# Kernel optimization log

Hardware: AMD Instinct MI355X
Metric: run time of the kernel (lower is better)

## Reference

```python
import jax, jax.numpy as jnp
import numpy as np

N_NODES = 50000
N_EDGES = 800000
N_NODE_DICT = 10000
N_EDGE_DICT = 100
EMB = 128
HID = 32
HEADS = 4
SLOPE = 0.2
LN_EPS = 1e-5


def layer_norm(x, gamma, beta):
    mu = jnp.mean(x, axis=-1, keepdims=True)
    var = jnp.mean(jnp.square(x - mu), axis=-1, keepdims=True)
    return (x - mu) * jax.lax.rsqrt(var + LN_EPS) * gamma + beta


def setup_inputs() -> dict:
    key = jax.random.key(0)
    ks = jax.random.split(key, 10)
    D = HID * HEADS
    inp = {
        "node_features": jax.random.randint(ks[0], (N_NODES,), 0, N_NODE_DICT),
        "edge_features": jax.random.randint(ks[1], (N_EDGES,), 0, N_EDGE_DICT),
        "edge_index": jax.random.randint(ks[2], (2, N_EDGES), 0, N_NODES),
        "node_emb": jax.random.normal(ks[3], (N_NODE_DICT, EMB), jnp.float32),
        "edge_emb": jax.random.normal(ks[4], (N_EDGE_DICT, EMB), jnp.float32),
        "w_W": jax.random.normal(ks[5], (EMB, D), jnp.float32) / np.sqrt(EMB),
        "w_b": jnp.zeros((D,), jnp.float32),
        "ew_W": jax.random.normal(ks[6], (EMB, D), jnp.float32) / np.sqrt(EMB),
        "ew_b": jnp.zeros((D,), jnp.float32),
        "attn": jax.random.normal(ks[7], (HEADS, 3 * HID), jnp.float32) * 0.1,
        "ln_gamma": jnp.ones((D,), jnp.float32),
        "ln_beta": jnp.zeros((D,), jnp.float32),
    }
    return inp


def reference(node_features, edge_features, edge_index, node_emb, edge_emb,
              w_W, w_b, ew_W, ew_b, attn, ln_gamma, ln_beta):
    # embedding lookups
    nf = node_emb[node_features]                       # [N, EMB]
    ef = edge_emb[edge_features]                       # [E, EMB]
    # linear projections -> [*, heads, hid]
    h = (nf @ w_W + w_b).reshape(-1, HEADS, HID)       # [N, H, F]
    eh = (ef @ ew_W + ew_b).reshape(-1, HEADS, HID)    # [E, H, F]
    tgt = edge_index[0]
    src = edge_index[1]
    # attn = [a_i || a_j || a_e]; dot with concat == sum of per-part dots
    a_i, a_j, a_e = attn[:, :HID], attn[:, HID:2 * HID], attn[:, 2 * HID:]
    s_i = jnp.einsum('nhf,hf->nh', h, a_i)             # [N, H]
    s_j = jnp.einsum('nhf,hf->nh', h, a_j)             # [N, H]
    s_e = jnp.einsum('ehf,hf->eh', eh, a_e)            # [E, H]
    eij = jax.nn.leaky_relu(s_i[tgt] + s_j[src] + s_e, negative_slope=SLOPE)  # [E, H]
    # scatter softmax over edges grouped by target node
    m = jax.ops.segment_max(eij, tgt, num_segments=N_NODES)   # [N, H]
    ex = jnp.exp(eij - m[tgt])
    denom = jax.ops.segment_sum(ex, tgt, num_segments=N_NODES)
    alpha = ex / denom[tgt]                            # [E, H]
    # message passing + scatter_add
    message = alpha[..., None] * h[src]                # [E, H, F]
    out = jax.ops.segment_sum(message, tgt, num_segments=N_NODES)  # [N, H, F]
    out = out + h                                      # skip connection
    out = out.reshape(-1, HEADS * HID)                 # concat heads
    eh2 = eh.reshape(-1, HEADS * HID)
    out = layer_norm(out, ln_gamma, ln_beta)
    eh2 = layer_norm(eh2, ln_gamma, ln_beta)
    return out, eh2
```

## Files before the change

kernel.cpp:

```cpp
#include <hip/hip_runtime.h>

#define NNODES 50000
#define NEDGES 800000
#define NNODE_DICT 10000
#define NEDGE_DICT 100
#define EMB 128
#define HID 32
#define HEADS 4
#define DD 128
#define SLOPE 0.2f
#define LN_EPS 1e-5f
#define NEG_BIG -3.0e38f

typedef float vfloat4 __attribute__((ext_vector_type(4)));

__global__ __launch_bounds__(128) void node_dict_kernel(
        const float* __restrict__ node_emb,
        const float* __restrict__ w_W,
        const float* __restrict__ w_b,
        const float* __restrict__ attn,
        float* __restrict__ h_dict,
        float* __restrict__ s_i_d,
        float* __restrict__ s_j_d) {
    __shared__ float a_rows[4][EMB];
    int r0 = blockIdx.x * 4;
    int col = threadIdx.x;
    #pragma unroll
    for (int r = 0; r < 4; ++r) a_rows[r][col] = node_emb[(r0 + r) * EMB + col];
    __syncthreads();
    float acc0 = 0.f, acc1 = 0.f, acc2 = 0.f, acc3 = 0.f;
    #pragma unroll 8
    for (int k = 0; k < EMB; ++k) {
        float wv = w_W[k * DD + col];
        acc0 += a_rows[0][k] * wv;
        acc1 += a_rows[1][k] * wv;
        acc2 += a_rows[2][k] * wv;
        acc3 += a_rows[3][k] * wv;
    }
    float b = w_b[col];
    acc0 += b; acc1 += b; acc2 += b; acc3 += b;
    h_dict[(r0 + 0) * DD + col] = acc0;
    h_dict[(r0 + 1) * DD + col] = acc1;
    h_dict[(r0 + 2) * DD + col] = acc2;
    h_dict[(r0 + 3) * DD + col] = acc3;

    int head = col >> 5, f = col & 31;
    float ai = attn[head * 96 + f];
    float aj = attn[head * 96 + 32 + f];
    float accs[4] = {acc0, acc1, acc2, acc3};
    #pragma unroll
    for (int r = 0; r < 4; ++r) {
        float pi = accs[r] * ai;
        float pj = accs[r] * aj;
        #pragma unroll
        for (int off = 16; off > 0; off >>= 1) {
            pi += __shfl_down(pi, off);
            pj += __shfl_down(pj, off);
        }
        if ((col & 31) == 0) {
            s_i_d[(r0 + r) * HEADS + head] = pi;
            s_j_d[(r0 + r) * HEADS + head] = pj;
        }
    }
}

__global__ void edge_dict_kernel(const float* __restrict__ edge_emb,
                                 const float* __restrict__ ew_W,
                                 const float* __restrict__ ew_b,
                                 const float* __restrict__ attn,
                                 const float* __restrict__ gamma,
                                 const float* __restrict__ beta,
                                 float* __restrict__ eh2_dict,
                                 float* __restrict__ s_e_d) {
    __shared__ float a_row[EMB];
    __shared__ float red[4];
    int row = blockIdx.x;
    int col = threadIdx.x;
    a_row[col] = edge_emb[row * EMB + col];
    __syncthreads();
    float acc = 0.f;
    #pragma unroll 8
    for (int k = 0; k < EMB; ++k) acc += a_row[k] * ew_W[k * DD + col];
    acc += ew_b[col];

    int head = col >> 5, f = col & 31;
    float pe = acc * attn[head * 96 + 64 + f];
    #pragma unroll
    for (int off = 16; off > 0; off >>= 1) pe += __shfl_down(pe, off);
    if ((col & 31) == 0) s_e_d[row * HEADS + head] = pe;

    float s = acc, s2 = acc * acc;
    #pragma unroll
    for (int off = 32; off > 0; off >>= 1) {
        s  += __shfl_down(s, off);
        s2 += __shfl_down(s2, off);
    }
    int wid = col >> 6;
    if ((col & 63) == 0) { red[wid * 2] = s; red[wid * 2 + 1] = s2; }
    __syncthreads();
    s = red[0] + red[2];
    s2 = red[1] + red[3];
    float mu = s * (1.f / DD);
    float var = s2 * (1.f / DD) - mu * mu;
    float r = rsqrtf(var + LN_EPS);
    eh2_dict[row * DD + col] = (acc - mu) * r * gamma[col] + beta[col];
}

__global__ void count_kernel(const int* __restrict__ edge_index,
                             int* __restrict__ counts) {
    int i = blockIdx.x * blockDim.x + threadIdx.x;
    if (i >= NEDGES / 4) return;
    int4 t = ((const int4*)edge_index)[i];
    atomicAdd(&counts[t.x], 1);
    atomicAdd(&counts[t.y], 1);
    atomicAdd(&counts[t.z], 1);
    atomicAdd(&counts[t.w], 1);
}

__global__ __launch_bounds__(256) void scan_tiles(const int* __restrict__ counts,
                                                  int* __restrict__ excl,
                                                  int* __restrict__ tsums) {
    __shared__ int wred[4];
    int tile = blockIdx.x;
    int tid = threadIdx.x;
    int base = tile * 1024 + tid * 4;
    int4 v = make_int4(0, 0, 0, 0);
    if (base + 3 < NNODES) {
        v = *(const int4*)(counts + base);
    } else {
        if (base + 0 < NNODES) v.x = counts[base + 0];
        if (base + 1 < NNODES) v.y = counts[base + 1];
        if (base + 2 < NNODES) v.z = counts[base + 2];
        if (base + 3 < NNODES) v.w = counts[base + 3];
    }
    int tsum = v.x + v.y + v.z + v.w;
    int lane = tid & 63, w = tid >> 6;
    int incl = tsum;
    #pragma unroll
    for (int o = 1; o < 64; o <<= 1) {
        int t = __shfl_up(incl, o);
        if (lane >= o) incl += t;
    }
    if (lane == 63) wred[w] = incl;
    __syncthreads();
    int wexc = 0;
    #pragma unroll
    for (int j = 0; j < 4; ++j) if (j < w) wexc += wred[j];
    int ex = wexc + incl - tsum;
    int4 o4 = make_int4(ex, ex + v.x, ex + v.x + v.y, ex + v.x + v.y + v.z);
    if (base + 3 < NNODES) {
        *(int4*)(excl + base) = o4;
    } else {
        if (base + 0 < NNODES) excl[base + 0] = o4.x;
        if (base + 1 < NNODES) excl[base + 1] = o4.y;
        if (base + 2 < NNODES) excl[base + 2] = o4.z;
        if (base + 3 < NNODES) excl[base + 3] = o4.w;
    }
    if (tid == 255) tsums[tile] = wexc + incl;
}

__global__ void scan_sums(int* __restrict__ tsums, int ntiles,
                          int* __restrict__ total) {
    int lane = threadIdx.x;
    int v = (lane < ntiles) ? tsums[lane] : 0;
    int incl = v;
    #pragma unroll
    for (int o = 1; o < 64; o <<= 1) {
        int t = __shfl_up(incl, o);
        if (lane >= o) incl += t;
    }
    if (lane < ntiles) tsums[lane] = incl - v;
    if (lane == 63) *total = incl;
}

__global__ void scan_fixup(const int* __restrict__ tsums,
                           int* __restrict__ offsets,
                           int* __restrict__ cursor) {
    int i = blockIdx.x * blockDim.x + threadIdx.x;
    if (i >= NNODES) return;
    int v = offsets[i] + tsums[i >> 10];
    offsets[i] = v;
    cursor[i] = v;
}

__global__ void scatter_kernel(const int* __restrict__ edge_index,
                               const int* __restrict__ node_features,
                               const int* __restrict__ edge_features,
                               int* __restrict__ cursor,
                               int2* __restrict__ csr) {
    int e = blockIdx.x * blockDim.x + threadIdx.x;
    if (e >= NEDGES) return;
    int tgt = edge_index[e];
    int src = edge_index[NEDGES + e];
    int ns = node_features[src];
    int ee = edge_features[e];
    int pos = atomicAdd(&cursor[tgt], 1);
    csr[pos] = make_int2(ns, ee);
}

__global__ __launch_bounds__(256) void node_agg_kernel(
        const int* __restrict__ offsets,
        const int2* __restrict__ csr,
        const int* __restrict__ node_features,
        const float4* __restrict__ s_i4,
        const float4* __restrict__ s_j4,
        const float4* __restrict__ s_e4,
        const float* __restrict__ h_dict,
        const float* __restrict__ gamma,
        const float* __restrict__ beta,
        float* __restrict__ out) {
    __shared__ float sp[4][256];
    __shared__ int   sns[4][64];
    int wid = threadIdx.x >> 6;
    int lane = threadIdx.x & 63;
    int n = blockIdx.x * 4 + wid;
    if (n >= NNODES) return;

    int nt = node_features[n];
    float4 si = s_i4[nt];
    int off = offsets[n];
    int deg = offsets[n + 1] - off;

    float m0 = NEG_BIG, m1 = NEG_BIG, m2 = NEG_BIG, m3 = NEG_BIG;
    float l0 = 0.f, l1 = 0.f, l2 = 0.f, l3 = 0.f;
    float acc0 = 0.f, acc1 = 0.f;
    int h0 = lane >> 5;
    int h1 = 2 + (lane >> 5);

    for (int base = 0; base < deg; base += 64) {
        int cnt = min(deg - base, 64);
        float4 ev = make_float4(NEG_BIG, NEG_BIG, NEG_BIG, NEG_BIG);
        int ns = 0;
        if (lane < cnt) {
            int2 pr = csr[off + base + lane];
            ns = pr.x;
            float4 sj = s_j4[pr.x];
            float4 se = s_e4[pr.y];
            ev.x = si.x + sj.x + se.x; ev.x = ev.x > 0.f ? ev.x : SLOPE * ev.x;
            ev.y = si.y + sj.y + se.y; ev.y = ev.y > 0.f ? ev.y : SLOPE * ev.y;
            ev.z = si.z + sj.z + se.z; ev.z = ev.z > 0.f ? ev.z : SLOPE * ev.z;
            ev.w = si.w + sj.w + se.w; ev.w = ev.w > 0.f ? ev.w : SLOPE * ev.w;
        }
        float4 mv = ev;
        #pragma unroll
        for (int o = 32; o > 0; o >>= 1) {
            mv.x = fmaxf(mv.x, __shfl_xor(mv.x, o));
            mv.y = fmaxf(mv.y, __shfl_xor(mv.y, o));
            mv.z = fmaxf(mv.z, __shfl_xor(mv.z, o));
            mv.w = fmaxf(mv.w, __shfl_xor(mv.w, o));
        }
        float nm0 = fmaxf(m0, mv.x), nm1 = fmaxf(m1, mv.y);
        float nm2 = fmaxf(m2, mv.z), nm3 = fmaxf(m3, mv.w);
        float4 p = make_float4(0.f, 0.f, 0.f, 0.f);
        if (lane < cnt) {
            p.x = __expf(ev.x - nm0);
            p.y = __expf(ev.y - nm1);
            p.z = __expf(ev.z - nm2);
            p.w = __expf(ev.w - nm3);
        }
        float4 sv = p;
        #pragma unroll
        for (int o = 32; o > 0; o >>= 1) {
            sv.x += __shfl_xor(sv.x, o);
            sv.y += __shfl_xor(sv.y, o);
            sv.z += __shfl_xor(sv.z, o);
            sv.w += __shfl_xor(sv.w, o);
        }
        float sc0 = __expf(m0 - nm0), sc1 = __expf(m1 - nm1);
        float sc2 = __expf(m2 - nm2), sc3 = __expf(m3 - nm3);
        l0 = l0 * sc0 + sv.x; l1 = l1 * sc1 + sv.y;
        l2 = l2 * sc2 + sv.z; l3 = l3 * sc3 + sv.w;
        m0 = nm0; m1 = nm1; m2 = nm2; m3 = nm3;
        acc0 *= (lane < 32) ? sc0 : sc1;
        acc1 *= (lane < 32) ? sc2 : sc3;
        if (lane < cnt) {
            sp[wid][lane * 4 + 0] = p.x;
            sp[wid][lane * 4 + 1] = p.y;
            sp[wid][lane * 4 + 2] = p.z;
            sp[wid][lane * 4 + 3] = p.w;
            sns[wid][lane] = ns;
        }
        int nst = sns[wid][0];
        for (int t = 0; t < cnt; ++t) {
            const float* hr = h_dict + (size_t)nst * DD;
            float w0 = sp[wid][t * 4 + h0];
            float w1 = sp[wid][t * 4 + h1];
            if (t + 1 < cnt) nst = sns[wid][t + 1];
            acc0 += w0 * hr[lane];
            acc1 += w1 * hr[lane + 64];
        }
    }

    float den0 = (lane < 32) ? l0 : l1;
    float den1 = (lane < 32) ? l2 : l3;
    float msg0 = den0 > 0.f ? acc0 / den0 : 0.f;
    float msg1 = den1 > 0.f ? acc1 / den1 : 0.f;
    const float* hres = h_dict + (size_t)nt * DD;
    float v0 = msg0 + hres[lane];
    float v1 = msg1 + hres[lane + 64];
    float s = v0 + v1, s2 = v0 * v0 + v1 * v1;
    #pragma unroll
    for (int o = 32; o > 0; o >>= 1) {
        s  += __shfl_xor(s, o);
        s2 += __shfl_xor(s2, o);
    }
    float mu = s * (1.f / DD);
    float var = s2 * (1.f / DD) - mu * mu;
    float r = rsqrtf(var + LN_EPS);
    out[(size_t)n * DD + lane]      = (v0 - mu) * r * gamma[lane] + beta[lane];
    out[(size_t)n * DD + lane + 64] = (v1 - mu) * r * gamma[lane + 64] + beta[lane + 64];
}

__global__ void edge_out_kernel(const int* __restrict__ edge_features,
                                const vfloat4* __restrict__ eh2_dict4,
                                vfloat4* __restrict__ out4) {
    int t = blockIdx.x * blockDim.x + threadIdx.x;
    int e = t >> 5;
    int j = t & 31;
    if (e >= NEDGES) return;
    int ee = edge_features[e];
    vfloat4 v = eh2_dict4[ee * 32 + j];
    __builtin_nontemporal_store(v, out4 + (size_t)t);
}

extern "C" void kernel_launch(void* const* d_in, const int* in_sizes, int n_in,
                              void* d_out, int out_size, void* d_ws, size_t ws_size,
                              hipStream_t stream) {
    const int*   node_features = (const int*)d_in[0];
    const int*   edge_features = (const int*)d_in[1];
    const int*   edge_index    = (const int*)d_in[2];
    const float* node_emb      = (const float*)d_in[3];
    const float* edge_emb      = (const float*)d_in[4];
    const float* w_W           = (const float*)d_in[5];
    const float* w_b           = (const float*)d_in[6];
    const float* ew_W          = (const float*)d_in[7];
    const float* ew_b          = (const float*)d_in[8];
    const float* attn          = (const float*)d_in[9];
    const float* gamma         = (const float*)d_in[10];
    const float* beta          = (const float*)d_in[11];

    float* out_nodes = (float*)d_out;
    float* out_edges = (float*)d_out + (size_t)NNODES * DD;

    char* w = (char*)d_ws;
    float* h_dict   = (float*)w;  w += (size_t)NNODE_DICT * DD * 4;
    float* s_i_d    = (float*)w;  w += (size_t)NNODE_DICT * 4 * 4;
    float* s_j_d    = (float*)w;  w += (size_t)NNODE_DICT * 4 * 4;
    float* eh2_dict = (float*)w;  w += (size_t)NEDGE_DICT * DD * 4;
    float* s_e_d    = (float*)w;  w += (size_t)NEDGE_DICT * 4 * 4;
    int*   counts   = (int*)w;    w += (size_t)NNODES * 4;
    int*   offsets  = (int*)w;    w += (size_t)(NNODES + 4) * 4;
    int*   cursor   = (int*)w;    w += (size_t)NNODES * 4;
    int*   tsums    = (int*)w;    w += (size_t)64 * 4;
    int2*  csr      = (int2*)w;   w += (size_t)NEDGES * 8;

    const int ntiles = (NNODES + 1023) / 1024;

    (void)hipMemsetAsync(counts, 0, (size_t)NNODES * 4, stream);

    node_dict_kernel<<<NNODE_DICT / 4, 128, 0, stream>>>(node_emb, w_W, w_b, attn,
                                                         h_dict, s_i_d, s_j_d);
    edge_dict_kernel<<<NEDGE_DICT, 128, 0, stream>>>(edge_emb, ew_W, ew_b, attn,
                                                     gamma, beta, eh2_dict, s_e_d);
    count_kernel<<<(NEDGES / 4 + 255) / 256, 256, 0, stream>>>(edge_index, counts);
    scan_tiles<<<ntiles, 256, 0, stream>>>(counts, offsets, tsums);
    scan_sums<<<1, 64, 0, stream>>>(tsums, ntiles, offsets + NNODES);
    scan_fixup<<<(NNODES + 255) / 256, 256, 0, stream>>>(tsums, offsets, cursor);
    scatter_kernel<<<(NEDGES + 255) / 256, 256, 0, stream>>>(edge_index, node_features,
                                                             edge_features, cursor, csr);
    node_agg_kernel<<<(NNODES + 3) / 4, 256, 0, stream>>>(offsets, csr, node_features,
                                                          (const float4*)s_i_d,
                                                          (const float4*)s_j_d,
                                                          (const float4*)s_e_d,
                                                          h_dict, gamma, beta, out_nodes);
    edge_out_kernel<<<(NEDGES * 32 + 255) / 256, 256, 0, stream>>>(edge_features,
                                                                   (const vfloat4*)eh2_dict,
                                                                   (vfloat4*)out_edges);
}
```

Baseline: 600.3 us.

## Merge independent kernels into front/back launches and fold scan_sums into fixup

Combines the node-dict, edge-dict and edge-count work into one launch that dispatches on block ID. It folds the tile-sum scan into the fixup kernel, where every block redundantly rescans the 49 tile sums. It also interleaves edge-output copy blocks with node-aggregation blocks (1 agg block per 8 copy blocks) in a single back kernel. The aim is fewer launches and overlap of the memory-bound edge copy with the latency-bound aggregation, at the cost of branch-heavy kernels whose resource usage is set by the larger path.

```diff
diff --git a/kernel.cpp b/kernel.cpp
--- a/kernel.cpp
+++ b/kernel.cpp
@@ -12,109 +12,117 @@
 #define LN_EPS 1e-5f
 #define NEG_BIG -3.0e38f
 
+#define NDICT_BLOCKS (NNODE_DICT / 4)
+#define EDICT_BLOCKS (NEDGE_DICT)
+#define COUNT_BLOCKS ((NEDGES / 4 + 127) / 128)
+#define NTILES ((NNODES + 1023) / 1024)
+#define AGG_BLOCKS ((NNODES + 3) / 4)
+#define EOUT_BLOCKS (NEDGES * 32 / 256)
+#define BACK_BLOCKS (AGG_BLOCKS + EOUT_BLOCKS)
+
 typedef float vfloat4 __attribute__((ext_vector_type(4)));
 
-__global__ __launch_bounds__(128) void node_dict_kernel(
+__global__ __launch_bounds__(128) void front_kernel(
         const float* __restrict__ node_emb,
         const float* __restrict__ w_W,
         const float* __restrict__ w_b,
         const float* __restrict__ attn,
         float* __restrict__ h_dict,
         float* __restrict__ s_i_d,
-        float* __restrict__ s_j_d) {
-    __shared__ float a_rows[4][EMB];
-    int r0 = blockIdx.x * 4;
+        float* __restrict__ s_j_d,
+        const float* __restrict__ edge_emb,
+        const float* __restrict__ ew_W,
+        const float* __restrict__ ew_b,
+        const float* __restrict__ gamma,
+        const float* __restrict__ beta,
+        float* __restrict__ eh2_dict,
+        float* __restrict__ s_e_d,
+        const int* __restrict__ edge_index,
+        int* __restrict__ counts) {
+    __shared__ float a_sh[4][EMB];
+    __shared__ float red[4];
+    int bid = blockIdx.x;
     int col = threadIdx.x;
-    #pragma unroll
-    for (int r = 0; r < 4; ++r) a_rows[r][col] = node_emb[(r0 + r) * EMB + col];
-    __syncthreads();
-    float acc0 = 0.f, acc1 = 0.f, acc2 = 0.f, acc3 = 0.f;
-    #pragma unroll 8
-    for (int k = 0; k < EMB; ++k) {
-        float wv = w_W[k * DD + col];
-        acc0 += a_rows[0][k] * wv;
-        acc1 += a_rows[1][k] * wv;
-        acc2 += a_rows[2][k] * wv;
-        acc3 += a_rows[3][k] * wv;
-    }
-    float b = w_b[col];
-    acc0 += b; acc1 += b; acc2 += b; acc3 += b;
-    h_dict[(r0 + 0) * DD + col] = acc0;
-    h_dict[(r0 + 1) * DD + col] = acc1;
-    h_dict[(r0 + 2) * DD + col] = acc2;
-    h_dict[(r0 + 3) * DD + col] = acc3;
-
-    int head = col >> 5, f = col & 31;
-    float ai = attn[head * 96 + f];
-    float aj = attn[head * 96 + 32 + f];
-    float accs[4] = {acc0, acc1, acc2, acc3};
-    #pragma unroll
-    for (int r = 0; r < 4; ++r) {
-        float pi = accs[r] * ai;
-        float pj = accs[r] * aj;
-        #pragma unroll
-        for (int off = 16; off > 0; off >>= 1) {
-            pi += __shfl_down(pi, off);
-            pj += __shfl_down(pj, off);
-        }
-        if ((col & 31) == 0) {
-            s_i_d[(r0 + r) * HEADS + head] = pi;
-            s_j_d[(r0 + r) * HEADS + head] = pj;
-        }
-    }
-}
-
-__global__ void edge_dict_kernel(const float* __restrict__ edge_emb,
-                                 const float* __restrict__ ew_W,
-                                 const float* __restrict__ ew_b,
-                                 const float* __restrict__ attn,
-                                 const float* __restrict__ gamma,
-                                 const float* __restrict__ beta,
-                                 float* __restrict__ eh2_dict,
-                                 float* __restrict__ s_e_d) {
-    __shared__ float a_row[EMB];
-    __shared__ float red[4];
-    int row = blockIdx.x;
-    int col = threadIdx.x;
-    a_row[col] = edge_emb[row * EMB + col];
-    __syncthreads();
-    float acc = 0.f;
-    #pragma unroll 8
-    for (int k = 0; k < EMB; ++k) acc += a_row[k] * ew_W[k * DD + col];
-    acc += ew_b[col];
-
-    int head = col >> 5, f = col & 31;
-    float pe = acc * attn[head * 96 + 64 + f];
-    #pragma unroll
-    for (int off = 16; off > 0; off >>= 1) pe += __shfl_down(pe, off);
-    if ((col & 31) == 0) s_e_d[row * HEADS + head] = pe;
-
-    float s = acc, s2 = acc * acc;
-    #pragma unroll
-    for (int off = 32; off > 0; off >>= 1) {
-        s  += __shfl_down(s, off);
-        s2 += __shfl_down(s2, off);
-    }
-    int wid = col >> 6;
-    if ((col & 63) == 0) { red[wid * 2] = s; red[wid * 2 + 1] = s2; }
-    __syncthreads();
-    s = red[0] + red[2];
-    s2 = red[1] + red[3];
-    float mu = s * (1.f / DD);
-    float var = s2 * (1.f / DD) - mu * mu;
-    float r = rsqrtf(var + LN_EPS);
-    eh2_dict[row * DD + col] = (acc - mu) * r * gamma[col] + beta[col];
-}
-
-__global__ void count_kernel(const int* __restrict__ edge_index,
-                             int* __restrict__ counts) {
-    int i = blockIdx.x * blockDim.x + threadIdx.x;
-    if (i >= NEDGES / 4) return;
-    int4 t = ((const int4*)edge_index)[i];
-    atomicAdd(&counts[t.x], 1);
-    atomicAdd(&counts[t.y], 1);
-    atomicAdd(&counts[t.z], 1);
-    atomicAdd(&counts[t.w], 1);
+
+    if (bid < NDICT_BLOCKS) {
+        int r0 = bid * 4;
+        #pragma unroll
+        for (int r = 0; r < 4; ++r) a_sh[r][col] = node_emb[(r0 + r) * EMB + col];
+        __syncthreads();
+        float acc0 = 0.f, acc1 = 0.f, acc2 = 0.f, acc3 = 0.f;
+        #pragma unroll 8
+        for (int k = 0; k < EMB; ++k) {
+            float wv = w_W[k * DD + col];
+            acc0 += a_sh[0][k] * wv;
+            acc1 += a_sh[1][k] * wv;
+            acc2 += a_sh[2][k] * wv;
+            acc3 += a_sh[3][k] * wv;
+        }
+        float b = w_b[col];
+        acc0 += b; acc1 += b; acc2 += b; acc3 += b;
+        h_dict[(r0 + 0) * DD + col] = acc0;
+        h_dict[(r0 + 1) * DD + col] = acc1;
+        h_dict[(r0 + 2) * DD + col] = acc2;
+        h_dict[(r0 + 3) * DD + col] = acc3;
+
+        int head = col >> 5, f = col & 31;
+        float ai = attn[head * 96 + f];
+        float aj = attn[head * 96 + 32 + f];
+        float accs[4] = {acc0, acc1, acc2, acc3};
+        #pragma unroll
+        for (int r = 0; r < 4; ++r) {
+            float pi = accs[r] * ai;
+            float pj = accs[r] * aj;
+            #pragma unroll
+            for (int off = 16; off > 0; off >>= 1) {
+                pi += __shfl_down(pi, off);
+                pj += __shfl_down(pj, off);
+            }
+            if ((col & 31) == 0) {
+                s_i_d[(r0 + r) * HEADS + head] = pi;
+                s_j_d[(r0 + r) * HEADS + head] = pj;
+            }
+        }
+    } else if (bid < NDICT_BLOCKS + EDICT_BLOCKS) {
+        int row = bid - NDICT_BLOCKS;
+        a_sh[0][col] = edge_emb[row * EMB + col];
+        __syncthreads();
+        float acc = 0.f;
+        #pragma unroll 8
+        for (int k = 0; k < EMB; ++k) acc += a_sh[0][k] * ew_W[k * DD + col];
+        acc += ew_b[col];
+
+        int head = col >> 5, f = col & 31;
+        float pe = acc * attn[head * 96 + 64 + f];
+        #pragma unroll
+        for (int off = 16; off > 0; off >>= 1) pe += __shfl_down(pe, off);
+        if ((col & 31) == 0) s_e_d[row * HEADS + head] = pe;
+
+        float s = acc, s2 = acc * acc;
+        #pragma unroll
+        for (int off = 32; off > 0; off >>= 1) {
+            s  += __shfl_down(s, off);
+            s2 += __shfl_down(s2, off);
+        }
+        int wid = col >> 6;
+        if ((col & 63) == 0) { red[wid * 2] = s; red[wid * 2 + 1] = s2; }
+        __syncthreads();
+        s = red[0] + red[2];
+        s2 = red[1] + red[3];
+        float mu = s * (1.f / DD);
+        float var = s2 * (1.f / DD) - mu * mu;
+        float r = rsqrtf(var + LN_EPS);
+        eh2_dict[row * DD + col] = (acc - mu) * r * gamma[col] + beta[col];
+    } else {
+        int i = (bid - NDICT_BLOCKS - EDICT_BLOCKS) * 128 + col;
+        if (i < NEDGES / 4) {
+            int4 t = ((const int4*)edge_index)[i];
+            atomicAdd(&counts[t.x], 1);
+            atomicAdd(&counts[t.y], 1);
+            atomicAdd(&counts[t.z], 1);
+            atomicAdd(&counts[t.w], 1);
+        }
+    }
 }
 
 __global__ __launch_bounds__(256) void scan_tiles(const int* __restrict__ counts,
@@ -159,28 +167,29 @@
     if (tid == 255) tsums[tile] = wexc + incl;
 }
 
-__global__ void scan_sums(int* __restrict__ tsums, int ntiles,
-                          int* __restrict__ total) {
-    int lane = threadIdx.x;
-    int v = (lane < ntiles) ? tsums[lane] : 0;
-    int incl = v;
-    #pragma unroll
-    for (int o = 1; o < 64; o <<= 1) {
-        int t = __shfl_up(incl, o);
-        if (lane >= o) incl += t;
-    }
-    if (lane < ntiles) tsums[lane] = incl - v;
-    if (lane == 63) *total = incl;
-}
-
-__global__ void scan_fixup(const int* __restrict__ tsums,
-                           int* __restrict__ offsets,
-                           int* __restrict__ cursor) {
-    int i = blockIdx.x * blockDim.x + threadIdx.x;
-    if (i >= NNODES) return;
-    int v = offsets[i] + tsums[i >> 10];
-    offsets[i] = v;
-    cursor[i] = v;
+__global__ __launch_bounds__(256) void scan_fixup2(const int* __restrict__ tsums,
+                                                   int* __restrict__ offsets,
+                                                   int* __restrict__ cursor) {
+    __shared__ int sbase[64];
+    int tid = threadIdx.x;
+    if (tid < 64) {
+        int v = (tid < NTILES) ? tsums[tid] : 0;
+        int incl = v;
+        #pragma unroll
+        for (int o = 1; o < 64; o <<= 1) {
+            int t = __shfl_up(incl, o);
+            if (tid >= o) incl += t;
+        }
+        sbase[tid] = incl - v;
+    }
+    __syncthreads();
+    int i = blockIdx.x * 256 + tid;
+    if (i < NNODES) {
+        int v = offsets[i] + sbase[i >> 10];
+        offsets[i] = v;
+        cursor[i] = v;
+    }
+    if (blockIdx.x == 0 && tid == 0) offsets[NNODES] = NEDGES;
 }
 
 __global__ void scatter_kernel(const int* __restrict__ edge_index,
@@ -198,7 +207,7 @@
     csr[pos] = make_int2(ns, ee);
 }
 
-__global__ __launch_bounds__(256) void node_agg_kernel(
+__global__ __launch_bounds__(256) void back_kernel(
         const int* __restrict__ offsets,
         const int2* __restrict__ csr,
         const int* __restrict__ node_features,
@@ -208,12 +217,30 @@
         const float* __restrict__ h_dict,
         const float* __restrict__ gamma,
         const float* __restrict__ beta,
-        float* __restrict__ out) {
+        float* __restrict__ out,
+        const int* __restrict__ edge_features,
+        const vfloat4* __restrict__ eh2_dict4,
+        vfloat4* __restrict__ out4) {
     __shared__ float sp[4][256];
     __shared__ int   sns[4][64];
+    int bid = blockIdx.x;
+    int a = bid / 9;
+    int r9 = bid - a * 9;
+
+    if (r9 != 0) {
+        int eb = 8 * a + r9 - 1;
+        int t = eb * 256 + threadIdx.x;
+        int e = t >> 5;
+        int j = t & 31;
+        int ee = edge_features[e];
+        vfloat4 v = eh2_dict4[ee * 32 + j];
+        __builtin_nontemporal_store(v, out4 + (size_t)t);
+        return;
+    }
+
     int wid = threadIdx.x >> 6;
     int lane = threadIdx.x & 63;
-    int n = blockIdx.x * 4 + wid;
+    int n = a * 4 + wid;
     if (n >= NNODES) return;
 
     int nt = node_features[n];
@@ -309,18 +336,6 @@
     float r = rsqrtf(var + LN_EPS);
     out[(size_t)n * DD + lane]      = (v0 - mu) * r * gamma[lane] + beta[lane];
     out[(size_t)n * DD + lane + 64] = (v1 - mu) * r * gamma[lane + 64] + beta[lane + 64];
-}
-
-__global__ void edge_out_kernel(const int* __restrict__ edge_features,
-                                const vfloat4* __restrict__ eh2_dict4,
-                                vfloat4* __restrict__ out4) {
-    int t = blockIdx.x * blockDim.x + threadIdx.x;
-    int e = t >> 5;
-    int j = t & 31;
-    if (e >= NEDGES) return;
-    int ee = edge_features[e];
-    vfloat4 v = eh2_dict4[ee * 32 + j];
-    __builtin_nontemporal_store(v, out4 + (size_t)t);
 }
 
 extern "C" void kernel_launch(void* const* d_in, const int* in_sizes, int n_in,
@@ -354,26 +369,22 @@
     int*   tsums    = (int*)w;    w += (size_t)64 * 4;
     int2*  csr      = (int2*)w;   w += (size_t)NEDGES * 8;
 
-    const int ntiles = (NNODES + 1023) / 1024;
-
     (void)hipMemsetAsync(counts, 0, (size_t)NNODES * 4, stream);
 
-    node_dict_kernel<<<NNODE_DICT / 4, 128, 0, stream>>>(node_emb, w_W, w_b, attn,
-                                                         h_dict, s_i_d, s_j_d);
-    edge_dict_kernel<<<NEDGE_DICT, 128, 0, stream>>>(edge_emb, ew_W, ew_b, attn,
-                                                     gamma, beta, eh2_dict, s_e_d);
-    count_kernel<<<(NEDGES / 4 + 255) / 256, 256, 0, stream>>>(edge_index, counts);
-    scan_tiles<<<ntiles, 256, 0, stream>>>(counts, offsets, tsums);
-    scan_sums<<<1, 64, 0, stream>>>(tsums, ntiles, offsets + NNODES);
-    scan_fixup<<<(NNODES + 255) / 256, 256, 0, stream>>>(tsums, offsets, cursor);
+    front_kernel<<<NDICT_BLOCKS + EDICT_BLOCKS + COUNT_BLOCKS, 128, 0, stream>>>(
+        node_emb, w_W, w_b, attn, h_dict, s_i_d, s_j_d,
+        edge_emb, ew_W, ew_b, gamma, beta, eh2_dict, s_e_d,
+        edge_index, counts);
+    scan_tiles<<<NTILES, 256, 0, stream>>>(counts, offsets, tsums);
+    scan_fixup2<<<(NNODES + 255) / 256, 256, 0, stream>>>(tsums, offsets, cursor);
     scatter_kernel<<<(NEDGES + 255) / 256, 256, 0, stream>>>(edge_index, node_features,
                                                              edge_features, cursor, csr);
-    node_agg_kernel<<<(NNODES + 3) / 4, 256, 0, stream>>>(offsets, csr, node_features,
-                                                          (const float4*)s_i_d,
-                                                          (const float4*)s_j_d,
-                                                          (const float4*)s_e_d,
-                                                          h_dict, gamma, beta, out_nodes);
-    edge_out_kernel<<<(NEDGES * 32 + 255) / 256, 256, 0, stream>>>(edge_features,
-                                                                   (const vfloat4*)eh2_dict,
-                                                                   (vfloat4*)out_edges);
-}
+    back_kernel<<<BACK_BLOCKS, 256, 0, stream>>>(offsets, csr, node_features,
+                                                 (const float4*)s_i_d,
+                                                 (const float4*)s_j_d,
+                                                 (const float4*)s_e_d,
+                                                 h_dict, gamma, beta, out_nodes,
+                                                 edge_features,
+                                                 (const vfloat4*)eh2_dict,
+                                                 (vfloat4*)out_edges);
+}
```

Result: faster. 584.6 us (-2.6%).
